# Optimization experiments

Hardware: AMD Instinct MI355X
Metric: run time of the kernel (lower is better)

## Reference

```python
import jax, jax.numpy as jnp
import numpy as np

A, NL, LD, F, W, DEPTH = 128, 16, 256, 256, 1024, 4
CH, CHD = 8, 64   # cross-attn heads / head_dim
SH, SHD = 8, 32   # latent self-attn heads / head_dim
FF = 256          # 2**ceil(log2(latent_dim))
FLAT = NL * LD


def _ln(x, g, b, eps=1e-5):
    m = x.mean(-1, keepdims=True)
    v = ((x - m) ** 2).mean(-1, keepdims=True)
    return (x - m) * jax.lax.rsqrt(v + eps) * g + b


def _attn(q_in, kv, wq, wk, wv, wo, bo, h, hd):
    b, s, _ = q_in.shape
    t = kv.shape[1]
    q = (q_in @ wq.T).reshape(b, s, h, hd)
    k = (kv @ wk.T).reshape(b, t, h, hd)
    v = (kv @ wv.T).reshape(b, t, h, hd)
    p = jax.nn.softmax(jnp.einsum('bihd,bjhd->bhij', q, k) * (hd ** -0.5), axis=-1)
    o = jnp.einsum('bhij,bjhd->bihd', p, v).reshape(b, s, h * hd)
    return o @ wo.T + bo


def _block(q, kv, p, h, hd):
    wq, wk, wv, wo, bo, g1, b1, fw1, fb1, fw2, fb2, g2, b2 = p
    z = _ln(q + _attn(q, kv, wq, wk, wv, wo, bo, h, hd), g1, b1)
    ff = jax.nn.relu(z @ fw1.T + fb1) @ fw2.T + fb2
    return _ln(z + ff, g2, b2)


def setup_inputs() -> dict:
    key = jax.random.key(0)
    ks = iter(jax.random.split(key, 40))
    def rn(shape, s=0.02):
        return jax.random.normal(next(ks), shape, jnp.float32) * s
    return {
        'x': jax.random.normal(next(ks), (A, W, F), jnp.float32),
        'z': jax.random.normal(next(ks), (A, NL, LD), jnp.float32),
        'c_wq': rn((CH * CHD, LD)), 'c_wk': rn((CH * CHD, F)), 'c_wv': rn((CH * CHD, F)),
        'c_wo': rn((LD, CH * CHD)), 'c_bo': jnp.zeros((LD,), jnp.float32),
        'c_ln1_g': jnp.ones((LD,), jnp.float32), 'c_ln1_b': jnp.zeros((LD,), jnp.float32),
        'c_ff_w1': rn((FF, LD)), 'c_ff_b1': jnp.zeros((FF,), jnp.float32),
        'c_ff_w2': rn((LD, FF)), 'c_ff_b2': jnp.zeros((LD,), jnp.float32),
        'c_ln2_g': jnp.ones((LD,), jnp.float32), 'c_ln2_b': jnp.zeros((LD,), jnp.float32),
        's_wq': rn((DEPTH, SH * SHD, LD)), 's_wk': rn((DEPTH, SH * SHD, LD)),
        's_wv': rn((DEPTH, SH * SHD, LD)), 's_wo': rn((DEPTH, LD, SH * SHD)),
        's_bo': jnp.zeros((DEPTH, LD), jnp.float32),
        's_ln1_g': jnp.ones((DEPTH, LD), jnp.float32), 's_ln1_b': jnp.zeros((DEPTH, LD), jnp.float32),
        's_ff_w1': rn((DEPTH, FF, LD)), 's_ff_b1': jnp.zeros((DEPTH, FF), jnp.float32),
        's_ff_w2': rn((DEPTH, LD, FF)), 's_ff_b2': jnp.zeros((DEPTH, LD), jnp.float32),
        's_ln2_g': jnp.ones((DEPTH, LD), jnp.float32), 's_ln2_b': jnp.zeros((DEPTH, LD), jnp.float32),
        'q_w': rn((FLAT, FLAT)), 'q_b': jnp.zeros((FLAT,), jnp.float32),
        'k_w': rn((FLAT, FLAT)), 'k_b': jnp.zeros((FLAT,), jnp.float32),
        'v_w': rn((FLAT, FLAT)), 'v_b': jnp.zeros((FLAT,), jnp.float32),
    }


def reference(x, z, c_wq, c_wk, c_wv, c_wo, c_bo, c_ln1_g, c_ln1_b, c_ff_w1, c_ff_b1,
              c_ff_w2, c_ff_b2, c_ln2_g, c_ln2_b,
              s_wq, s_wk, s_wv, s_wo, s_bo, s_ln1_g, s_ln1_b, s_ff_w1, s_ff_b1,
              s_ff_w2, s_ff_b2, s_ln2_g, s_ln2_b,
              q_w, q_b, k_w, k_b, v_w, v_b):
    z_prior = z
    # NOTE: original LSRE.forward computes cross-attention but assigns the
    # result to x and never uses it. Replicated faithfully (dead computation;
    # output does not depend on x or the cross-attn params).
    _ = _block(z, x, (c_wq, c_wk, c_wv, c_wo, c_bo, c_ln1_g, c_ln1_b,
                      c_ff_w1, c_ff_b1, c_ff_w2, c_ff_b2, c_ln2_g, c_ln2_b), CH, CHD)
    zc = z
    sp = (s_wq, s_wk, s_wv, s_wo, s_bo, s_ln1_g, s_ln1_b,
          s_ff_w1, s_ff_b1, s_ff_w2, s_ff_b2, s_ln2_g, s_ln2_b)
    for i in range(DEPTH):
        zc = _block(zc, zc, tuple(p[i] for p in sp), SH, SHD)
    # CANN: asset-to-asset attention; broadcast-mul-then-sum == attn @ v
    zf = zc.reshape(A, FLAT)
    q = zf @ q_w.T + q_b
    k = zf @ k_w.T + k_b
    v = zf @ v_w.T + v_b
    attn = jax.nn.softmax((q @ k.T) * (LD ** -0.5), axis=-1)
    h = (attn @ v).reshape(A, NL, LD)
    return (h, z_prior)
```

## Files before the change

kernel.cpp:

```cpp
#include <hip/hip_runtime.h>
#include <math.h>

typedef __bf16 bf16x8 __attribute__((ext_vector_type(8)));
typedef __bf16 bf16x4 __attribute__((ext_vector_type(4)));
typedef float  f32x4  __attribute__((ext_vector_type(4)));

#define MFMA(a,b,c) __builtin_amdgcn_mfma_f32_16x16x32_bf16((a),(b),(c),0,0,0)

#define A_N   128
#define LDIM  256
#define FLATD 4096

__global__ __launch_bounds__(256) void k_cvt_w(
        const float* __restrict__ s0, const float* __restrict__ s1,
        const float* __restrict__ s2, const float* __restrict__ s3,
        const float* __restrict__ s4, const float* __restrict__ s5,
        __bf16* __restrict__ W) {
    const int gid = blockIdx.x * 256 + threadIdx.x;
    const int m   = gid >> 15;
    const int rem = gid & 32767;
    const int off = rem << 3;
    const int lp  = off >> 16;
    const int win = off & 65535;
    const int row = win >> 8;
    const int c   = win & 255;
    const int w   = row >> 4, lr = row & 15;
    const int ks  = c >> 5,  q  = (c >> 3) & 3;
    const int lane = q * 16 + lr;

    int li_h;
    if (m < 3)       li_h = ks * 6 + m * 2;
    else if (m == 3) li_h = 48 + ks * 2;
    else if (m == 4) li_h = 64 + ks * 2;
    else             li_h = 80 + ks * 2;

    const float* s;
    switch (m) {
        case 0: s = s0; break; case 1: s = s1; break; case 2: s = s2; break;
        case 3: s = s3; break; case 4: s = s4; break; default: s = s5; break;
    }
    const float4* sp = (const float4*)(s + off);
    float4 x = sp[0], y = sp[1];
    float v[8] = {x.x, x.y, x.z, x.w, y.x, y.y, y.z, y.w};
    bf16x8 h, l;
    #pragma unroll
    for (int j = 0; j < 8; ++j) {
        __bf16 hh = (__bf16)v[j];
        h[j] = hh;
        l[j] = (__bf16)(v[j] - (float)hh);
    }
    __bf16* dst = W + (size_t)(lp * 16 + w) * 49152 + (size_t)lane * 8;
    *(bf16x8*)(dst + (size_t)li_h * 512)       = h;
    *(bf16x8*)(dst + (size_t)(li_h + 1) * 512) = l;
}

__global__ __launch_bounds__(1024) void k_latent(
    const float* __restrict__ z,
    const __bf16* __restrict__ Wswz,
    const float* __restrict__ boa,
    const float* __restrict__ g1a, const float* __restrict__ b1a,
    const float* __restrict__ fb1a, const float* __restrict__ fb2a,
    const float* __restrict__ g2a, const float* __restrict__ b2a,
    float* __restrict__ zprior, __bf16* __restrict__ Zbh, __bf16* __restrict__ Zbl)
{
    __shared__ __align__(16) char arena[57856];
    float*  zf  = (float*)arena;
    __bf16* zbh = (__bf16*)(arena + 16384);
    __bf16* zbl = (__bf16*)(arena + 24832);
    __bf16* Ph  = (__bf16*)(arena + 16384);
    __bf16* Qh  = (__bf16*)(arena + 33280);
    __bf16* ob  = Qh;
    __bf16* Kh  = (__bf16*)(arena + 41472);
    __bf16* Vt  = (__bf16*)(arena + 49664);

    const int a    = blockIdx.x;
    const int t    = threadIdx.x;
    const int w    = t >> 6;
    const int lane = t & 63;
    const int q    = lane >> 4;
    const int r    = lane & 15;
    const int nc   = w * 16;
    const int head = w >> 1;
    const int hc   = (w & 1) * 16;

    {
        int row = t >> 6, col = (t & 63) * 4;
        const float4 x = *(const float4*)(z + (size_t)a * 4096 + row * 256 + col);
        *(float4*)(zprior + (size_t)a * 4096 + row * 256 + col) = x;
        float v[4] = {x.x, x.y, x.z, x.w};
        float*  zr = zf  + row * 256 + col;
        __bf16* zh = zbh + row * 264 + col;
        __bf16* zl = zbl + row * 264 + col;
        #pragma unroll
        for (int j = 0; j < 4; ++j) {
            zr[j] = v[j];
            __bf16 hh = (__bf16)v[j];
            zh[j] = hh;
            zl[j] = (__bf16)(v[j] - (float)hh);
        }
    }
    __syncthreads();

    auto do_ln = [&](const float* g, const float* bb) {
        int col = lane * 4;
        float* zr = zf + w * 256 + col;
        float4 v4 = *(const float4*)zr;
        float v[4] = {v4.x, v4.y, v4.z, v4.w};
        float s1 = 0.f, s2 = 0.f;
        #pragma unroll
        for (int j = 0; j < 4; ++j) { s1 += v[j]; s2 += v[j]*v[j]; }
        #pragma unroll
        for (int o = 1; o <= 32; o <<= 1) {
            s1 += __shfl_xor(s1, o);
            s2 += __shfl_xor(s2, o);
        }
        float mean = s1 * (1.0f/256.0f);
        float var  = s2 * (1.0f/256.0f) - mean * mean;
        float inv  = rsqrtf(var + 1e-5f);
        float4 g4 = *(const float4*)(g + col);
        float4 b4 = *(const float4*)(bb + col);
        float gg[4] = {g4.x, g4.y, g4.z, g4.w};
        float bbv[4] = {b4.x, b4.y, b4.z, b4.w};
        __bf16* zh = zbh + w * 264 + col;
        __bf16* zl = zbl + w * 264 + col;
        float y[4];
        #pragma unroll
        for (int j = 0; j < 4; ++j) {
            y[j] = (v[j] - mean) * inv * gg[j] + bbv[j];
            __bf16 hh = (__bf16)y[j];
            zh[j] = hh;
            zl[j] = (__bf16)(y[j] - (float)hh);
        }
        *(float4*)zr = (float4){y[0], y[1], y[2], y[3]};
    };

    const f32x4 zero4 = {0.f, 0.f, 0.f, 0.f};
    bf16x8 zer8;
    #pragma unroll
    for (int j = 0; j < 8; ++j) zer8[j] = (__bf16)0.0f;

    for (int lp = 0; lp < 4; ++lp) {
        const float* bo  = boa  + lp*256;
        const float* g1  = g1a  + lp*256; const float* b1 = b1a + lp*256;
        const float* fb1 = fb1a + lp*256; const float* fb2 = fb2a + lp*256;
        const float* g2  = g2a  + lp*256; const float* b2 = b2a + lp*256;

        const __bf16* wsl = Wswz + (size_t)(lp * 16 + w) * 49152 + (size_t)lane * 8;
        #define WCHUNK(idx) (*(const bf16x8*)(wsl + (idx) * 512))

        const __bf16* zA_h = zbh + r * 264 + q * 8;
        const __bf16* zA_l = zbl + r * 264 + q * 8;
        const __bf16* oA   = ob  + r * 264 + q * 8;

        {
            f32x4 aq = zero4, ak = zero4, av = zero4;
            #pragma unroll
            for (int ks = 0; ks < 8; ++ks) {
                bf16x8 afh = *(const bf16x8*)(zA_h + ks*32);
                bf16x8 afl = *(const bf16x8*)(zA_l + ks*32);
                bf16x8 qh = WCHUNK(ks*6 + 0);
                bf16x8 ql = WCHUNK(ks*6 + 1);
                bf16x8 kh = WCHUNK(ks*6 + 2);
                bf16x8 kl = WCHUNK(ks*6 + 3);
                bf16x8 vh = WCHUNK(ks*6 + 4);
                bf16x8 vl = WCHUNK(ks*6 + 5);
                aq = MFMA(afh, qh, aq); aq = MFMA(afl, qh, aq); aq = MFMA(afh, ql, aq);
                ak = MFMA(afh, kh, ak); ak = MFMA(afl, kh, ak); ak = MFMA(afh, kl, ak);
                av = MFMA(afh, vh, av); av = MFMA(afl, vh, av); av = MFMA(afh, vl, av);
            }
            #pragma unroll
            for (int i = 0; i < 4; ++i) {
                int m = q*4 + i;
                Qh[(head*16 + m)*32 + hc + r] = (__bf16)aq[i];
                Kh[(head*16 + m)*32 + hc + r] = (__bf16)ak[i];
                Vt[(head*32 + hc + r)*16 + m] = (__bf16)av[i];
            }
        }
        __syncthreads();

        if (w < 8) {
            bf16x8 qa = *(const bf16x8*)(Qh + (w*16 + r)*32 + q*8);
            bf16x8 ka = *(const bf16x8*)(Kh + (w*16 + r)*32 + q*8);
            f32x4 s = MFMA(qa, ka, zero4);
            #pragma unroll
            for (int i = 0; i < 4; ++i) {
                float sc = s[i] * 0.17677669529663687f;
                float mx = sc;
                #pragma unroll
                for (int o = 1; o <= 8; o <<= 1) mx = fmaxf(mx, __shfl_xor(mx, o, 16));
                float e = __expf(sc - mx);
                float sm = e;
                #pragma unroll
                for (int o = 1; o <= 8; o <<= 1) sm += __shfl_xor(sm, o, 16);
                Ph[(w*16 + q*4 + i)*32 + r]      = (__bf16)(e / sm);
                Ph[(w*16 + q*4 + i)*32 + 16 + r] = (__bf16)0.0f;
            }
        }
        __syncthreads();

        {
            int ph = w & 7, vnt = w >> 3;
            bf16x8 pa = *(const bf16x8*)(Ph + (ph*16 + r)*32 + q*8);
            bf16x8 vb = (q < 2)
                ? *(const bf16x8*)(Vt + (ph*32 + vnt*16 + r)*16 + q*8) : zer8;
            f32x4 o = MFMA(pa, vb, zero4);
            #pragma unroll
            for (int i = 0; i < 4; ++i)
                ob[(q*4 + i)*264 + ph*32 + vnt*16 + r] = (__bf16)o[i];
        }
        __syncthreads();

        {
            f32x4 acc = zero4;
            #pragma unroll
            for (int ks = 0; ks < 8; ++ks) {
                bf16x8 af = *(const bf16x8*)(oA + ks*32);
                bf16x8 bh = WCHUNK(48 + ks*2);
                bf16x8 bl = WCHUNK(49 + ks*2);
                acc = MFMA(af, bh, acc);
                acc = MFMA(af, bl, acc);
            }
            #pragma unroll
            for (int i = 0; i < 4; ++i) {
                int row = q*4 + i, col = nc + r;
                zf[row*256 + col] = acc[i] + bo[col] + zf[row*256 + col];
            }
        }
        __syncthreads();
        do_ln(g1, b1);
        __syncthreads();

        {
            f32x4 acc = zero4;
            #pragma unroll
            for (int ks = 0; ks < 8; ++ks) {
                bf16x8 afh = *(const bf16x8*)(zA_h + ks*32);
                bf16x8 afl = *(const bf16x8*)(zA_l + ks*32);
                bf16x8 bh  = WCHUNK(64 + ks*2);
                bf16x8 bl  = WCHUNK(65 + ks*2);
                acc = MFMA(afh, bh, acc);
                acc = MFMA(afl, bh, acc);
                acc = MFMA(afh, bl, acc);
            }
            #pragma unroll
            for (int i = 0; i < 4; ++i) {
                int row = q*4 + i, col = nc + r;
                ob[row*264 + col] = (__bf16)fmaxf(acc[i] + fb1[col], 0.0f);
            }
        }
        __syncthreads();

        {
            f32x4 acc = zero4;
            #pragma unroll
            for (int ks = 0; ks < 8; ++ks) {
                bf16x8 af = *(const bf16x8*)(oA + ks*32);
                bf16x8 bh = WCHUNK(80 + ks*2);
                bf16x8 bl = WCHUNK(81 + ks*2);
                acc = MFMA(af, bh, acc);
                acc = MFMA(af, bl, acc);
            }
            #pragma unroll
            for (int i = 0; i < 4; ++i) {
                int row = q*4 + i, col = nc + r;
                zf[row*256 + col] = acc[i] + fb2[col] + zf[row*256 + col];
            }
        }
        __syncthreads();
        do_ln(g2, b2);
        __syncthreads();
        #undef WCHUNK
    }

    {
        int row = t >> 6, col = (t & 63) * 4;
        *(bf16x4*)(Zbh + (size_t)a * 4096 + row * 256 + col) =
            *(const bf16x4*)(zbh + row * 264 + col);
        *(bf16x4*)(Zbl + (size_t)a * 4096 + row * 256 + col) =
            *(const bf16x4*)(zbl + row * 264 + col);
    }
}

__global__ __launch_bounds__(512) void k_cann_gemm(
    const __bf16* __restrict__ Zh, const __bf16* __restrict__ Zl,
    const float* __restrict__ W0, const float* __restrict__ W1, const float* __restrict__ W2,
    const float* __restrict__ b0, const float* __restrict__ b1, const float* __restrict__ b2,
    float* __restrict__ C0, float* __restrict__ C1, float* __restrict__ C2)
{
    const float* W; const float* bias; float* C;
    if (blockIdx.y == 0)      { W = W0; bias = b0; C = C0; }
    else if (blockIdx.y == 1) { W = W1; bias = b1; C = C1; }
    else                      { W = W2; bias = b2; C = C2; }

    __shared__ __bf16 AshB[2][128 * 72];
    __shared__ __bf16 AslB[2][128 * 72];
    __shared__ __bf16 BshB[2][64 * 72];
    __shared__ __bf16 BslB[2][64 * 72];

    const int t = threadIdx.x;
    const int w = t >> 6, lane = t & 63, q = lane >> 4, r = lane & 15;
    const int n0 = blockIdx.x * 64;
    const int m0 = (w >> 1) * 32;
    const int nw = (w & 1) * 32;

    const int ar0 = t >> 3, ac = (t & 7) * 8;
    const int br  = t >> 3, bc = (t & 7) * 8;

    struct Stage { bf16x8 a0h, a1h, a0l, a1l; f32x4 wx, wy; };

    auto issue = [&](Stage& S, int k0) {
        S.a0h = __builtin_nontemporal_load(
                    (const bf16x8*)(Zh + (size_t)ar0        * FLATD + k0 + ac));
        S.a1h = __builtin_nontemporal_load(
                    (const bf16x8*)(Zh + (size_t)(ar0 + 64) * FLATD + k0 + ac));
        S.a0l = __builtin_nontemporal_load(
                    (const bf16x8*)(Zl + (size_t)ar0        * FLATD + k0 + ac));
        S.a1l = __builtin_nontemporal_load(
                    (const bf16x8*)(Zl + (size_t)(ar0 + 64) * FLATD + k0 + ac));
        const f32x4* wp = (const f32x4*)(W + (size_t)(n0 + br) * FLATD + k0 + bc);
        S.wx = __builtin_nontemporal_load(wp);
        S.wy = __builtin_nontemporal_load(wp + 1);
    };

    auto wr = [&](const Stage& S, int b) {
        *(bf16x8*)(&AshB[b][ar0 * 72 + ac])        = S.a0h;
        *(bf16x8*)(&AshB[b][(ar0 + 64) * 72 + ac]) = S.a1h;
        *(bf16x8*)(&AslB[b][ar0 * 72 + ac])        = S.a0l;
        *(bf16x8*)(&AslB[b][(ar0 + 64) * 72 + ac]) = S.a1l;
        float v[8] = {S.wx[0], S.wx[1], S.wx[2], S.wx[3],
                      S.wy[0], S.wy[1], S.wy[2], S.wy[3]};
        bf16x8 h, l;
        #pragma unroll
        for (int j = 0; j < 8; ++j) {
            __bf16 hh = (__bf16)v[j];
            h[j] = hh;
            l[j] = (__bf16)(v[j] - (float)hh);
        }
        *(bf16x8*)(&BshB[b][br * 72 + bc]) = h;
        *(bf16x8*)(&BslB[b][br * 72 + bc]) = l;
    };

    const f32x4 zero4 = {0.f, 0.f, 0.f, 0.f};
    f32x4 acc[2][2] = {{zero4, zero4}, {zero4, zero4}};

    auto mfma_phase = [&](int b) {
        #pragma unroll
        for (int ks = 0; ks < 2; ++ks) {
            bf16x8 a0h = *(const bf16x8*)(&AshB[b][(m0 + r)      * 72 + ks*32 + q*8]);
            bf16x8 a1h = *(const bf16x8*)(&AshB[b][(m0 + 16 + r) * 72 + ks*32 + q*8]);
            bf16x8 a0l = *(const bf16x8*)(&AslB[b][(m0 + r)      * 72 + ks*32 + q*8]);
            bf16x8 a1l = *(const bf16x8*)(&AslB[b][(m0 + 16 + r) * 72 + ks*32 + q*8]);
            bf16x8 g0h = *(const bf16x8*)(&BshB[b][(nw + r)      * 72 + ks*32 + q*8]);
            bf16x8 g1h = *(const bf16x8*)(&BshB[b][(nw + 16 + r) * 72 + ks*32 + q*8]);
            bf16x8 g0l = *(const bf16x8*)(&BslB[b][(nw + r)      * 72 + ks*32 + q*8]);
            bf16x8 g1l = *(const bf16x8*)(&BslB[b][(nw + 16 + r) * 72 + ks*32 + q*8]);
            acc[0][0] = MFMA(a0h, g0h, acc[0][0]);
            acc[0][0] = MFMA(a0l, g0h, acc[0][0]);
            acc[0][0] = MFMA(a0h, g0l, acc[0][0]);
            acc[0][1] = MFMA(a0h, g1h, acc[0][1]);
            acc[0][1] = MFMA(a0l, g1h, acc[0][1]);
            acc[0][1] = MFMA(a0h, g1l, acc[0][1]);
            acc[1][0] = MFMA(a1h, g0h, acc[1][0]);
            acc[1][0] = MFMA(a1l, g0h, acc[1][0]);
            acc[1][0] = MFMA(a1h, g0l, acc[1][0]);
            acc[1][1] = MFMA(a1h, g1h, acc[1][1]);
            acc[1][1] = MFMA(a1l, g1h, acc[1][1]);
            acc[1][1] = MFMA(a1h, g1l, acc[1][1]);
        }
    };

    #define LGKM0_BAR() do {                                      \
        asm volatile("s_waitcnt lgkmcnt(0)" ::: "memory");        \
        __builtin_amdgcn_sched_barrier(0);                        \
        __builtin_amdgcn_s_barrier();                             \
        __builtin_amdgcn_sched_barrier(0);                        \
    } while (0)

    Stage S0, S1;
    issue(S0, 0);
    issue(S1, 64);
    wr(S0, 0);
    LGKM0_BAR();

    int cur = 0;
    int kk  = 128;
    for (int it = 0; it < 31; ++it) {
        issue(S0, kk); kk += 64;
        mfma_phase(cur);
        wr(S1, cur ^ 1);
        LGKM0_BAR();
        cur ^= 1;
        issue(S1, kk); kk += 64;
        mfma_phase(cur);
        wr(S0, cur ^ 1);
        LGKM0_BAR();
        cur ^= 1;
    }
    mfma_phase(cur);
    wr(S1, cur ^ 1);
    LGKM0_BAR();
    cur ^= 1;
    mfma_phase(cur);
    #undef LGKM0_BAR

    if (blockIdx.y == 1) {
        #pragma unroll
        for (int mi = 0; mi < 2; ++mi)
            #pragma unroll
            for (int ni = 0; ni < 2; ++ni)
                #pragma unroll
                for (int i = 0; i < 4; ++i) {
                    int row = m0 + mi*16 + q*4 + i;
                    int col = n0 + nw + ni*16 + r;
                    C[(size_t)col * 128 + row] = acc[mi][ni][i] + bias[col];
                }
    } else {
        #pragma unroll
        for (int mi = 0; mi < 2; ++mi)
            #pragma unroll
            for (int ni = 0; ni < 2; ++ni)
                #pragma unroll
                for (int i = 0; i < 4; ++i) {
                    int row = m0 + mi*16 + q*4 + i;
                    int col = n0 + nw + ni*16 + r;
                    C[(size_t)row * FLATD + col] = acc[mi][ni][i] + bias[col];
                }
    }
}

__global__ __launch_bounds__(512) void k_cann_scores(const float* __restrict__ Q,
                              const float* __restrict__ KT,
                              float* __restrict__ P) {
    const int i0 = blockIdx.x * 2;
    const int t  = threadIdx.x;
    __shared__ float qs[2][FLATD];
    __shared__ float part[4][2][128];
    __shared__ float wred[2][2];
    __shared__ float wsum[2][2];
    {
        const float4* src = (const float4*)(Q + (size_t)i0 * FLATD);
        float4* dst = (float4*)qs;
        #pragma unroll
        for (int u = 0; u < 4; ++u) dst[t + u * 512] = src[t + u * 512];
    }
    __syncthreads();

    const int j = t & 127, ksub = t >> 7;
    const float* kp = KT + (size_t)(ksub * 1024) * 128 + j;
    const float* q0 = qs[0] + ksub * 1024;
    const float* q1 = qs[1] + ksub * 1024;
    float a0 = 0.0f, a1 = 0.0f;
    #pragma unroll 8
    for (int k = 0; k < 1024; ++k) {
        float kv = kp[(size_t)k * 128];
        a0 += q0[k] * kv;
        a1 += q1[k] * kv;
    }
    part[ksub][0][j] = a0;
    part[ksub][1][j] = a1;
    __syncthreads();

    float v = 0.0f, e = 0.0f;
    const int i = t >> 7;
    if (t < 256)
        v = (part[0][i][j] + part[1][i][j] + part[2][i][j] + part[3][i][j]) * 0.0625f;

    float mx = (t < 256) ? v : -3.4e38f;
    #pragma unroll
    for (int o = 32; o; o >>= 1) mx = fmaxf(mx, __shfl_xor(mx, o));
    if (t < 256 && (j & 63) == 0) wred[i][j >> 6] = mx;
    __syncthreads();
    if (t < 256) {
        mx = fmaxf(wred[i][0], wred[i][1]);
        e = __expf(v - mx);
    }
    float sum = e;
    #pragma unroll
    for (int o = 32; o; o >>= 1) sum += __shfl_xor(sum, o);
    if (t < 256 && (j & 63) == 0) wsum[i][j >> 6] = sum;
    __syncthreads();
    if (t < 256) {
        sum = wsum[i][0] + wsum[i][1];
        P[(size_t)(i0 + i) * 128 + j] = e / sum;
    }
}

__global__ __launch_bounds__(256) void k_cann_out(const float* __restrict__ P,
                           const float* __restrict__ V,
                           float* __restrict__ H) {
    const int i0 = blockIdx.y * 8;
    const int t  = threadIdx.x;
    const int nb = blockIdx.x * 1024 + t * 4;
    __shared__ float ps[128][8];
    #pragma unroll
    for (int u = 0; u < 4; ++u) {
        int e = t + u * 256;
        int i = e >> 7, j = e & 127;
        ps[j][i] = P[(size_t)(i0 + i) * 128 + j];
    }
    __syncthreads();

    f32x4 acc[8];
    #pragma unroll
    for (int i = 0; i < 8; ++i) acc[i] = (f32x4){0.f, 0.f, 0.f, 0.f};

    for (int j = 0; j < 128; ++j) {
        float4 vv = *(const float4*)(V + (size_t)j * FLATD + nb);
        f32x4 v4 = {vv.x, vv.y, vv.z, vv.w};
        float4 pa = *(const float4*)&ps[j][0];
        float4 pb = *(const float4*)&ps[j][4];
        acc[0] += pa.x * v4; acc[1] += pa.y * v4;
        acc[2] += pa.z * v4; acc[3] += pa.w * v4;
        acc[4] += pb.x * v4; acc[5] += pb.y * v4;
        acc[6] += pb.z * v4; acc[7] += pb.w * v4;
    }
    #pragma unroll
    for (int i = 0; i < 8; ++i) {
        f32x4 a = acc[i];
        *(float4*)(H + (size_t)(i0 + i) * FLATD + nb) =
            (float4){a[0], a[1], a[2], a[3]};
    }
}

extern "C" void kernel_launch(void* const* d_in, const int* in_sizes, int n_in,
                              void* d_out, int out_size, void* d_ws, size_t ws_size,
                              hipStream_t stream) {
    (void)in_sizes; (void)n_in; (void)out_size; (void)ws_size;

    const float* z      = (const float*)d_in[1];
    const float* s_wq   = (const float*)d_in[15];
    const float* s_wk   = (const float*)d_in[16];
    const float* s_wv   = (const float*)d_in[17];
    const float* s_wo   = (const float*)d_in[18];
    const float* s_bo   = (const float*)d_in[19];
    const float* s_ln1g = (const float*)d_in[20];
    const float* s_ln1b = (const float*)d_in[21];
    const float* s_fw1  = (const float*)d_in[22];
    const float* s_fb1  = (const float*)d_in[23];
    const float* s_fw2  = (const float*)d_in[24];
    const float* s_fb2  = (const float*)d_in[25];
    const float* s_ln2g = (const float*)d_in[26];
    const float* s_ln2b = (const float*)d_in[27];
    const float* q_w    = (const float*)d_in[28];
    const float* q_b    = (const float*)d_in[29];
    const float* k_w    = (const float*)d_in[30];
    const float* k_b    = (const float*)d_in[31];
    const float* v_w    = (const float*)d_in[32];
    const float* v_b    = (const float*)d_in[33];

    float* out    = (float*)d_out;
    float* Hout   = out;
    float* Zprior = out + 524288;

    char* w8 = (char*)d_ws;
    __bf16* Wswz = (__bf16*)w8;
    float*  Qb  = (float*)w8;
    float*  Kb  = (float*)(w8 + 2097152);
    float*  Vb  = (float*)(w8 + 4194304);
    __bf16* Zbh = (__bf16*)(w8 + 6291456);
    __bf16* Zbl = (__bf16*)(w8 + 7340032);
    float*  Pm  = (float*)(w8 + 8388608);

    k_cvt_w<<<768, 256, 0, stream>>>(s_wq, s_wk, s_wv, s_wo, s_fw1, s_fw2, Wswz);

    k_latent<<<A_N, 1024, 0, stream>>>(z, Wswz, s_bo, s_ln1g, s_ln1b,
                                       s_fb1, s_fb2, s_ln2g, s_ln2b,
                                       Zprior, Zbh, Zbl);

    k_cann_gemm<<<dim3(FLATD / 64, 3), 512, 0, stream>>>(Zbh, Zbl, q_w, k_w, v_w,
                                                         q_b, k_b, v_b, Qb, Kb, Vb);

    k_cann_scores<<<A_N / 2, 512, 0, stream>>>(Qb, Kb, Pm);
    k_cann_out<<<dim3(4, 16), 256, 0, stream>>>(Pm, Vb, Hout);
}
```

Baseline: 514.2 us.

## Store latent Z in MFMA-fragment layout and load A operands directly to registers

k_latent now writes the bf16 hi/lo latent output in a pre-swizzled layout that matches the MFMA A-fragment order. The CANN projection GEMM then loads A fragments straight from global memory into registers, with no LDS staging, which cuts its LDS footprint and traffic. The loop is reordered so MFMAs run on the current registers while the next tile's loads are issued. Each wave now loads its own A fragments, so waves sharing a row group fetch duplicate data and register pressure goes up.

```diff
diff --git a/kernel.cpp b/kernel.cpp
--- a/kernel.cpp
+++ b/kernel.cpp
@@ -61,7 +61,7 @@
     const float* __restrict__ g1a, const float* __restrict__ b1a,
     const float* __restrict__ fb1a, const float* __restrict__ fb2a,
     const float* __restrict__ g2a, const float* __restrict__ b2a,
-    float* __restrict__ zprior, __bf16* __restrict__ Zbh, __bf16* __restrict__ Zbl)
+    float* __restrict__ zprior, __bf16* __restrict__ Zsh, __bf16* __restrict__ Zsl)
 {
     __shared__ __align__(16) char arena[57856];
     float*  zf  = (float*)arena;
@@ -272,17 +272,17 @@
         #undef WCHUNK
     }
 
-    {
-        int row = t >> 6, col = (t & 63) * 4;
-        *(bf16x4*)(Zbh + (size_t)a * 4096 + row * 256 + col) =
-            *(const bf16x4*)(zbh + row * 264 + col);
-        *(bf16x4*)(Zbl + (size_t)a * 4096 + row * 256 + col) =
-            *(const bf16x4*)(zbl + row * 264 + col);
+    if (t < 512) {
+        int srow = t >> 5, scol = (t & 31) * 8;
+        size_t dest = ((size_t)((a >> 4) * 128 + (t >> 2)) << 9)
+                    + (size_t)(((t & 3) * 16 + (a & 15)) * 8);
+        *(bf16x8*)(Zsh + dest) = *(const bf16x8*)(zbh + srow * 264 + scol);
+        *(bf16x8*)(Zsl + dest) = *(const bf16x8*)(zbl + srow * 264 + scol);
     }
 }
 
 __global__ __launch_bounds__(512) void k_cann_gemm(
-    const __bf16* __restrict__ Zh, const __bf16* __restrict__ Zl,
+    const __bf16* __restrict__ Zsh, const __bf16* __restrict__ Zsl,
     const float* __restrict__ W0, const float* __restrict__ W1, const float* __restrict__ W2,
     const float* __restrict__ b0, const float* __restrict__ b1, const float* __restrict__ b2,
     float* __restrict__ C0, float* __restrict__ C1, float* __restrict__ C2)
@@ -292,8 +292,6 @@
     else if (blockIdx.y == 1) { W = W1; bias = b1; C = C1; }
     else                      { W = W2; bias = b2; C = C2; }
 
-    __shared__ __bf16 AshB[2][128 * 72];
-    __shared__ __bf16 AslB[2][128 * 72];
     __shared__ __bf16 BshB[2][64 * 72];
     __shared__ __bf16 BslB[2][64 * 72];
 
@@ -302,33 +300,32 @@
     const int n0 = blockIdx.x * 64;
     const int m0 = (w >> 1) * 32;
     const int nw = (w & 1) * 32;
-
-    const int ar0 = t >> 3, ac = (t & 7) * 8;
-    const int br  = t >> 3, bc = (t & 7) * 8;
-
-    struct Stage { bf16x8 a0h, a1h, a0l, a1l; f32x4 wx, wy; };
-
-    auto issue = [&](Stage& S, int k0) {
-        S.a0h = __builtin_nontemporal_load(
-                    (const bf16x8*)(Zh + (size_t)ar0        * FLATD + k0 + ac));
-        S.a1h = __builtin_nontemporal_load(
-                    (const bf16x8*)(Zh + (size_t)(ar0 + 64) * FLATD + k0 + ac));
-        S.a0l = __builtin_nontemporal_load(
-                    (const bf16x8*)(Zl + (size_t)ar0        * FLATD + k0 + ac));
-        S.a1l = __builtin_nontemporal_load(
-                    (const bf16x8*)(Zl + (size_t)(ar0 + 64) * FLATD + k0 + ac));
-        const f32x4* wp = (const f32x4*)(W + (size_t)(n0 + br) * FLATD + k0 + bc);
-        S.wx = __builtin_nontemporal_load(wp);
-        S.wy = __builtin_nontemporal_load(wp + 1);
+    const int g0 = (w >> 1) * 2;
+    const int br = t >> 3, bc = (t & 7) * 8;
+
+    bf16x8 Ah0[2][2], Al0[2][2];
+    bf16x8 Ah1[2][2], Al1[2][2];
+    f32x4  Wx0, Wy0, Wx1, Wy1;
+
+    auto issue = [&](bf16x8 (&Ah)[2][2], bf16x8 (&Al)[2][2],
+                     f32x4& Wx, f32x4& Wy, int tile) {
+        const f32x4* wp = (const f32x4*)(W + (size_t)(n0 + br) * FLATD
+                                           + tile * 64 + bc);
+        Wx = __builtin_nontemporal_load(wp);
+        Wy = __builtin_nontemporal_load(wp + 1);
+        #pragma unroll
+        for (int gi = 0; gi < 2; ++gi)
+            #pragma unroll
+            for (int ks = 0; ks < 2; ++ks) {
+                size_t off = ((size_t)((g0 + gi) * 128 + tile * 2 + ks) << 9)
+                           + (size_t)(lane * 8);
+                Ah[gi][ks] = __builtin_nontemporal_load((const bf16x8*)(Zsh + off));
+                Al[gi][ks] = __builtin_nontemporal_load((const bf16x8*)(Zsl + off));
+            }
     };
 
-    auto wr = [&](const Stage& S, int b) {
-        *(bf16x8*)(&AshB[b][ar0 * 72 + ac])        = S.a0h;
-        *(bf16x8*)(&AshB[b][(ar0 + 64) * 72 + ac]) = S.a1h;
-        *(bf16x8*)(&AslB[b][ar0 * 72 + ac])        = S.a0l;
-        *(bf16x8*)(&AslB[b][(ar0 + 64) * 72 + ac]) = S.a1l;
-        float v[8] = {S.wx[0], S.wx[1], S.wx[2], S.wx[3],
-                      S.wy[0], S.wy[1], S.wy[2], S.wy[3]};
+    auto wrB = [&](const f32x4& Wx, const f32x4& Wy, int b) {
+        float v[8] = {Wx[0], Wx[1], Wx[2], Wx[3], Wy[0], Wy[1], Wy[2], Wy[3]};
         bf16x8 h, l;
         #pragma unroll
         for (int j = 0; j < 8; ++j) {
@@ -343,29 +340,26 @@
     const f32x4 zero4 = {0.f, 0.f, 0.f, 0.f};
     f32x4 acc[2][2] = {{zero4, zero4}, {zero4, zero4}};
 
-    auto mfma_phase = [&](int b) {
+    auto mfma_phase = [&](const bf16x8 (&Ah)[2][2], const bf16x8 (&Al)[2][2],
+                          int b) {
         #pragma unroll
         for (int ks = 0; ks < 2; ++ks) {
-            bf16x8 a0h = *(const bf16x8*)(&AshB[b][(m0 + r)      * 72 + ks*32 + q*8]);
-            bf16x8 a1h = *(const bf16x8*)(&AshB[b][(m0 + 16 + r) * 72 + ks*32 + q*8]);
-            bf16x8 a0l = *(const bf16x8*)(&AslB[b][(m0 + r)      * 72 + ks*32 + q*8]);
-            bf16x8 a1l = *(const bf16x8*)(&AslB[b][(m0 + 16 + r) * 72 + ks*32 + q*8]);
             bf16x8 g0h = *(const bf16x8*)(&BshB[b][(nw + r)      * 72 + ks*32 + q*8]);
             bf16x8 g1h = *(const bf16x8*)(&BshB[b][(nw + 16 + r) * 72 + ks*32 + q*8]);
             bf16x8 g0l = *(const bf16x8*)(&BslB[b][(nw + r)      * 72 + ks*32 + q*8]);
             bf16x8 g1l = *(const bf16x8*)(&BslB[b][(nw + 16 + r) * 72 + ks*32 + q*8]);
-            acc[0][0] = MFMA(a0h, g0h, acc[0][0]);
-            acc[0][0] = MFMA(a0l, g0h, acc[0][0]);
-            acc[0][0] = MFMA(a0h, g0l, acc[0][0]);
-            acc[0][1] = MFMA(a0h, g1h, acc[0][1]);
-            acc[0][1] = MFMA(a0l, g1h, acc[0][1]);
-            acc[0][1] = MFMA(a0h, g1l, acc[0][1]);
-            acc[1][0] = MFMA(a1h, g0h, acc[1][0]);
-            acc[1][0] = MFMA(a1l, g0h, acc[1][0]);
-            acc[1][0] = MFMA(a1h, g0l, acc[1][0]);
-            acc[1][1] = MFMA(a1h, g1h, acc[1][1]);
-            acc[1][1] = MFMA(a1l, g1h, acc[1][1]);
-            acc[1][1] = MFMA(a1h, g1l, acc[1][1]);
+            acc[0][0] = MFMA(Ah[0][ks], g0h, acc[0][0]);
+            acc[0][0] = MFMA(Al[0][ks], g0h, acc[0][0]);
+            acc[0][0] = MFMA(Ah[0][ks], g0l, acc[0][0]);
+            acc[0][1] = MFMA(Ah[0][ks], g1h, acc[0][1]);
+            acc[0][1] = MFMA(Al[0][ks], g1h, acc[0][1]);
+            acc[0][1] = MFMA(Ah[0][ks], g1l, acc[0][1]);
+            acc[1][0] = MFMA(Ah[1][ks], g0h, acc[1][0]);
+            acc[1][0] = MFMA(Al[1][ks], g0h, acc[1][0]);
+            acc[1][0] = MFMA(Ah[1][ks], g0l, acc[1][0]);
+            acc[1][1] = MFMA(Ah[1][ks], g1h, acc[1][1]);
+            acc[1][1] = MFMA(Al[1][ks], g1h, acc[1][1]);
+            acc[1][1] = MFMA(Ah[1][ks], g1l, acc[1][1]);
         }
     };
 
@@ -376,31 +370,25 @@
         __builtin_amdgcn_sched_barrier(0);                        \
     } while (0)
 
-    Stage S0, S1;
-    issue(S0, 0);
-    issue(S1, 64);
-    wr(S0, 0);
+    issue(Ah0, Al0, Wx0, Wy0, 0);
+    issue(Ah1, Al1, Wx1, Wy1, 1);
+    wrB(Wx0, Wy0, 0);
     LGKM0_BAR();
 
-    int cur = 0;
-    int kk  = 128;
     for (int it = 0; it < 31; ++it) {
-        issue(S0, kk); kk += 64;
-        mfma_phase(cur);
-        wr(S1, cur ^ 1);
+        mfma_phase(Ah0, Al0, 0);
+        issue(Ah0, Al0, Wx0, Wy0, 2*it + 2);
+        wrB(Wx1, Wy1, 1);
         LGKM0_BAR();
-        cur ^= 1;
-        issue(S1, kk); kk += 64;
-        mfma_phase(cur);
-        wr(S0, cur ^ 1);
+        mfma_phase(Ah1, Al1, 1);
+        issue(Ah1, Al1, Wx1, Wy1, 2*it + 3);
+        wrB(Wx0, Wy0, 0);
         LGKM0_BAR();
-        cur ^= 1;
-    }
-    mfma_phase(cur);
-    wr(S1, cur ^ 1);
+    }
+    mfma_phase(Ah0, Al0, 0);
+    wrB(Wx1, Wy1, 1);
     LGKM0_BAR();
-    cur ^= 1;
-    mfma_phase(cur);
+    mfma_phase(Ah1, Al1, 1);
     #undef LGKM0_BAR
 
     if (blockIdx.y == 1) {
@@ -557,17 +545,17 @@
     float*  Qb  = (float*)w8;
     float*  Kb  = (float*)(w8 + 2097152);
     float*  Vb  = (float*)(w8 + 4194304);
-    __bf16* Zbh = (__bf16*)(w8 + 6291456);
-    __bf16* Zbl = (__bf16*)(w8 + 7340032);
+    __bf16* Zsh = (__bf16*)(w8 + 6291456);
+    __bf16* Zsl = (__bf16*)(w8 + 7340032);
     float*  Pm  = (float*)(w8 + 8388608);
 
     k_cvt_w<<<768, 256, 0, stream>>>(s_wq, s_wk, s_wv, s_wo, s_fw1, s_fw2, Wswz);
 
     k_latent<<<A_N, 1024, 0, stream>>>(z, Wswz, s_bo, s_ln1g, s_ln1b,
                                        s_fb1, s_fb2, s_ln2g, s_ln2b,
-                                       Zprior, Zbh, Zbl);
-
-    k_cann_gemm<<<dim3(FLATD / 64, 3), 512, 0, stream>>>(Zbh, Zbl, q_w, k_w, v_w,
+                                       Zprior, Zsh, Zsl);
+
+    k_cann_gemm<<<dim3(FLATD / 64, 3), 512, 0, stream>>>(Zsh, Zsl, q_w, k_w, v_w,
                                                          q_b, k_b, v_b, Qb, Kb, Vb);
 
     k_cann_scores<<<A_N / 2, 512, 0, stream>>>(Qb, Kb, Pm);
```

New measurement: 533.2 us. +3.7%, slower.

## Halve CANN GEMM N-tile and drop LDS double buffering for more blocks

Applied to the files above, without the earlier changes.

The CANN projection GEMM tile shrinks from 64 to 32 output columns, doubling the grid from 192 to 384 blocks so more CUs are busy. The LDS double buffer and two-stage register prefetch become a single buffer with one prefetch stage and an extra barrier per k-step. This aims to fix under-occupancy of the large-weight GEMM, at the cost of re-reading the Z activations twice as often and exposing more barrier latency.

```diff
diff --git a/kernel.cpp b/kernel.cpp
--- a/kernel.cpp
+++ b/kernel.cpp
@@ -292,80 +292,70 @@
     else if (blockIdx.y == 1) { W = W1; bias = b1; C = C1; }
     else                      { W = W2; bias = b2; C = C2; }
 
-    __shared__ __bf16 AshB[2][128 * 72];
-    __shared__ __bf16 AslB[2][128 * 72];
-    __shared__ __bf16 BshB[2][64 * 72];
-    __shared__ __bf16 BslB[2][64 * 72];
+    __shared__ __bf16 Ash[128 * 72];
+    __shared__ __bf16 Asl[128 * 72];
+    __shared__ __bf16 Bsh[32 * 72];
+    __shared__ __bf16 Bsl[32 * 72];
 
     const int t = threadIdx.x;
     const int w = t >> 6, lane = t & 63, q = lane >> 4, r = lane & 15;
-    const int n0 = blockIdx.x * 64;
+    const int n0 = blockIdx.x * 32;
     const int m0 = (w >> 1) * 32;
-    const int nw = (w & 1) * 32;
+    const int nw = (w & 1) * 16;
 
     const int ar0 = t >> 3, ac = (t & 7) * 8;
-    const int br  = t >> 3, bc = (t & 7) * 8;
-
-    struct Stage { bf16x8 a0h, a1h, a0l, a1l; f32x4 wx, wy; };
-
-    auto issue = [&](Stage& S, int k0) {
+    const int br  = t >> 4, bc = (t & 15) * 4;
+
+    struct Stage { bf16x8 a0h, a1h, a0l, a1l; f32x4 wv; };
+    Stage S;
+
+    auto issue = [&](int k0) {
+        S.wv = __builtin_nontemporal_load(
+                   (const f32x4*)(W + (size_t)(n0 + br) * FLATD + k0 + bc));
         S.a0h = __builtin_nontemporal_load(
-                    (const bf16x8*)(Zh + (size_t)ar0        * FLATD + k0 + ac));
+                   (const bf16x8*)(Zh + (size_t)ar0        * FLATD + k0 + ac));
         S.a1h = __builtin_nontemporal_load(
-                    (const bf16x8*)(Zh + (size_t)(ar0 + 64) * FLATD + k0 + ac));
+                   (const bf16x8*)(Zh + (size_t)(ar0 + 64) * FLATD + k0 + ac));
         S.a0l = __builtin_nontemporal_load(
-                    (const bf16x8*)(Zl + (size_t)ar0        * FLATD + k0 + ac));
+                   (const bf16x8*)(Zl + (size_t)ar0        * FLATD + k0 + ac));
         S.a1l = __builtin_nontemporal_load(
-                    (const bf16x8*)(Zl + (size_t)(ar0 + 64) * FLATD + k0 + ac));
-        const f32x4* wp = (const f32x4*)(W + (size_t)(n0 + br) * FLATD + k0 + bc);
-        S.wx = __builtin_nontemporal_load(wp);
-        S.wy = __builtin_nontemporal_load(wp + 1);
+                   (const bf16x8*)(Zl + (size_t)(ar0 + 64) * FLATD + k0 + ac));
     };
 
-    auto wr = [&](const Stage& S, int b) {
-        *(bf16x8*)(&AshB[b][ar0 * 72 + ac])        = S.a0h;
-        *(bf16x8*)(&AshB[b][(ar0 + 64) * 72 + ac]) = S.a1h;
-        *(bf16x8*)(&AslB[b][ar0 * 72 + ac])        = S.a0l;
-        *(bf16x8*)(&AslB[b][(ar0 + 64) * 72 + ac]) = S.a1l;
-        float v[8] = {S.wx[0], S.wx[1], S.wx[2], S.wx[3],
-                      S.wy[0], S.wy[1], S.wy[2], S.wy[3]};
-        bf16x8 h, l;
-        #pragma unroll
-        for (int j = 0; j < 8; ++j) {
-            __bf16 hh = (__bf16)v[j];
+    auto wr = [&]() {
+        *(bf16x8*)(&Ash[ar0 * 72 + ac])        = S.a0h;
+        *(bf16x8*)(&Ash[(ar0 + 64) * 72 + ac]) = S.a1h;
+        *(bf16x8*)(&Asl[ar0 * 72 + ac])        = S.a0l;
+        *(bf16x8*)(&Asl[(ar0 + 64) * 72 + ac]) = S.a1l;
+        bf16x4 h, l;
+        #pragma unroll
+        for (int j = 0; j < 4; ++j) {
+            __bf16 hh = (__bf16)S.wv[j];
             h[j] = hh;
-            l[j] = (__bf16)(v[j] - (float)hh);
-        }
-        *(bf16x8*)(&BshB[b][br * 72 + bc]) = h;
-        *(bf16x8*)(&BslB[b][br * 72 + bc]) = l;
+            l[j] = (__bf16)(S.wv[j] - (float)hh);
+        }
+        *(bf16x4*)(&Bsh[br * 72 + bc]) = h;
+        *(bf16x4*)(&Bsl[br * 72 + bc]) = l;
     };
 
     const f32x4 zero4 = {0.f, 0.f, 0.f, 0.f};
-    f32x4 acc[2][2] = {{zero4, zero4}, {zero4, zero4}};
-
-    auto mfma_phase = [&](int b) {
+    f32x4 acc0 = zero4, acc1 = zero4;
+
+    auto mfma_phase = [&]() {
         #pragma unroll
         for (int ks = 0; ks < 2; ++ks) {
-            bf16x8 a0h = *(const bf16x8*)(&AshB[b][(m0 + r)      * 72 + ks*32 + q*8]);
-            bf16x8 a1h = *(const bf16x8*)(&AshB[b][(m0 + 16 + r) * 72 + ks*32 + q*8]);
-            bf16x8 a0l = *(const bf16x8*)(&AslB[b][(m0 + r)      * 72 + ks*32 + q*8]);
-            bf16x8 a1l = *(const bf16x8*)(&AslB[b][(m0 + 16 + r) * 72 + ks*32 + q*8]);
-            bf16x8 g0h = *(const bf16x8*)(&BshB[b][(nw + r)      * 72 + ks*32 + q*8]);
-            bf16x8 g1h = *(const bf16x8*)(&BshB[b][(nw + 16 + r) * 72 + ks*32 + q*8]);
-            bf16x8 g0l = *(const bf16x8*)(&BslB[b][(nw + r)      * 72 + ks*32 + q*8]);
-            bf16x8 g1l = *(const bf16x8*)(&BslB[b][(nw + 16 + r) * 72 + ks*32 + q*8]);
-            acc[0][0] = MFMA(a0h, g0h, acc[0][0]);
-            acc[0][0] = MFMA(a0l, g0h, acc[0][0]);
-            acc[0][0] = MFMA(a0h, g0l, acc[0][0]);
-            acc[0][1] = MFMA(a0h, g1h, acc[0][1]);
-            acc[0][1] = MFMA(a0l, g1h, acc[0][1]);
-            acc[0][1] = MFMA(a0h, g1l, acc[0][1]);
-            acc[1][0] = MFMA(a1h, g0h, acc[1][0]);
-            acc[1][0] = MFMA(a1l, g0h, acc[1][0]);
-            acc[1][0] = MFMA(a1h, g0l, acc[1][0]);
-            acc[1][1] = MFMA(a1h, g1h, acc[1][1]);
-            acc[1][1] = MFMA(a1l, g1h, acc[1][1]);
-            acc[1][1] = MFMA(a1h, g1l, acc[1][1]);
+            bf16x8 a0h = *(const bf16x8*)(&Ash[(m0 + r)      * 72 + ks*32 + q*8]);
+            bf16x8 a1h = *(const bf16x8*)(&Ash[(m0 + 16 + r) * 72 + ks*32 + q*8]);
+            bf16x8 a0l = *(const bf16x8*)(&Asl[(m0 + r)      * 72 + ks*32 + q*8]);
+            bf16x8 a1l = *(const bf16x8*)(&Asl[(m0 + 16 + r) * 72 + ks*32 + q*8]);
+            bf16x8 gh  = *(const bf16x8*)(&Bsh[(nw + r)      * 72 + ks*32 + q*8]);
+            bf16x8 gl  = *(const bf16x8*)(&Bsl[(nw + r)      * 72 + ks*32 + q*8]);
+            acc0 = MFMA(a0h, gh, acc0);
+            acc0 = MFMA(a0l, gh, acc0);
+            acc0 = MFMA(a0h, gl, acc0);
+            acc1 = MFMA(a1h, gh, acc1);
+            acc1 = MFMA(a1l, gh, acc1);
+            acc1 = MFMA(a1h, gl, acc1);
         }
     };
 
@@ -376,55 +366,38 @@
         __builtin_amdgcn_sched_barrier(0);                        \
     } while (0)
 
-    Stage S0, S1;
-    issue(S0, 0);
-    issue(S1, 64);
-    wr(S0, 0);
+    issue(0);
+    wr();
     LGKM0_BAR();
 
-    int cur = 0;
-    int kk  = 128;
-    for (int it = 0; it < 31; ++it) {
-        issue(S0, kk); kk += 64;
-        mfma_phase(cur);
-        wr(S1, cur ^ 1);
+    for (int tl = 0; tl < 63; ++tl) {
+        issue((tl + 1) * 64);
+        mfma_phase();
         LGKM0_BAR();
-        cur ^= 1;
-        issue(S1, kk); kk += 64;
-        mfma_phase(cur);
-        wr(S0, cur ^ 1);
+        wr();
         LGKM0_BAR();
-        cur ^= 1;
-    }
-    mfma_phase(cur);
-    wr(S1, cur ^ 1);
-    LGKM0_BAR();
-    cur ^= 1;
-    mfma_phase(cur);
+    }
+    mfma_phase();
     #undef LGKM0_BAR
 
     if (blockIdx.y == 1) {
         #pragma unroll
-        for (int mi = 0; mi < 2; ++mi)
-            #pragma unroll
-            for (int ni = 0; ni < 2; ++ni)
-                #pragma unroll
-                for (int i = 0; i < 4; ++i) {
-                    int row = m0 + mi*16 + q*4 + i;
-                    int col = n0 + nw + ni*16 + r;
-                    C[(size_t)col * 128 + row] = acc[mi][ni][i] + bias[col];
-                }
+        for (int i = 0; i < 4; ++i) {
+            int col = n0 + nw + r;
+            int row0 = m0 + q*4 + i;
+            int row1 = m0 + 16 + q*4 + i;
+            C[(size_t)col * 128 + row0] = acc0[i] + bias[col];
+            C[(size_t)col * 128 + row1] = acc1[i] + bias[col];
+        }
     } else {
         #pragma unroll
-        for (int mi = 0; mi < 2; ++mi)
-            #pragma unroll
-            for (int ni = 0; ni < 2; ++ni)
-                #pragma unroll
-                for (int i = 0; i < 4; ++i) {
-                    int row = m0 + mi*16 + q*4 + i;
-                    int col = n0 + nw + ni*16 + r;
-                    C[(size_t)row * FLATD + col] = acc[mi][ni][i] + bias[col];
-                }
+        for (int i = 0; i < 4; ++i) {
+            int col = n0 + nw + r;
+            int row0 = m0 + q*4 + i;
+            int row1 = m0 + 16 + q*4 + i;
+            C[(size_t)row0 * FLATD + col] = acc0[i] + bias[col];
+            C[(size_t)row1 * FLATD + col] = acc1[i] + bias[col];
+        }
     }
 }
 
@@ -567,7 +540,7 @@
                                        s_fb1, s_fb2, s_ln2g, s_ln2b,
                                        Zprior, Zbh, Zbl);
 
-    k_cann_gemm<<<dim3(FLATD / 64, 3), 512, 0, stream>>>(Zbh, Zbl, q_w, k_w, v_w,
+    k_cann_gemm<<<dim3(FLATD / 32, 3), 512, 0, stream>>>(Zbh, Zbl, q_w, k_w, v_w,
                                                          q_b, k_b, v_b, Qb, Kb, Vb);
 
     k_cann_scores<<<A_N / 2, 512, 0, stream>>>(Qb, Kb, Pm);
```

New measurement: 539.0 us. 1.05x slower.
